# Kernel tuning notes

Hardware: AMD Instinct MI355X
Metric: run time of the kernel (lower is better)

Reference implementation:

```python
import jax, jax.numpy as jnp
import numpy as np

G, NPG, C, H, F, L = 256, 128, 16, 128, 128, 3
N = G * NPG          # 32768 nodes
E = 524288           # 16 edges per node on average
REG, REG_C = 0.01, 0.01
LN_EPS = 1e-5


def setup_inputs() -> dict:
    key = jax.random.key(0)
    ks = jax.random.split(key, 20)
    x = jax.random.normal(ks[0], (N, F), dtype=jnp.float32)
    # edges kept within each graph so dense pooling matches to_dense_batch semantics
    epg = E // G
    offs = jnp.repeat(jnp.arange(G, dtype=jnp.int64) * NPG, epg)
    src = jax.random.randint(ks[1], (E,), 0, NPG, dtype=jnp.int64) + offs
    tgt = jax.random.randint(ks[2], (E,), 0, NPG, dtype=jnp.int64) + offs
    edge_index = jnp.stack([src, tgt])
    mask_breaks = jax.random.bernoulli(ks[3], 0.5, (E,))
    s = jax.random.uniform(ks[4], (N, C), dtype=jnp.float32)
    batch = jnp.repeat(jnp.arange(G, dtype=jnp.int64), NPG)
    sc = 1.0 / np.sqrt(H)
    Wn = jax.random.normal(ks[5], (L, H, H), dtype=jnp.float32) * sc
    bn_ = jax.random.normal(ks[6], (L, H), dtype=jnp.float32) * sc
    Wo = jax.random.normal(ks[7], (L, H, H), dtype=jnp.float32) * sc
    bo = jax.random.normal(ks[8], (L, H), dtype=jnp.float32) * sc
    Wr = jax.random.normal(ks[9], (L, H, H), dtype=jnp.float32) * sc
    ln_g = jnp.ones((L, H), dtype=jnp.float32)
    ln_b = jnp.zeros((L, H), dtype=jnp.float32)
    fln_g = jnp.ones((H,), dtype=jnp.float32)
    fln_b = jnp.zeros((H,), dtype=jnp.float32)
    lin_w = jax.random.normal(ks[10], (1, H), dtype=jnp.float32) * sc
    bias = jnp.zeros((1,), dtype=jnp.float32)
    return {"x": x, "edge_index": edge_index, "mask_breaks": mask_breaks, "s": s,
            "batch": batch, "Wn": Wn, "bn_": bn_, "Wo": Wo, "bo": bo, "Wr": Wr,
            "ln_g": ln_g, "ln_b": ln_b, "fln_g": fln_g, "fln_b": fln_b,
            "lin_w": lin_w, "bias": bias}


def _layernorm(h, g, b):
    mu = jnp.mean(h, axis=-1, keepdims=True)
    v = jnp.mean(jnp.square(h - mu), axis=-1, keepdims=True)
    return (h - mu) * jax.lax.rsqrt(v + LN_EPS) * g + b


def reference(x, edge_index, mask_breaks, s, batch, Wn, bn_, Wo, bo, Wr,
              ln_g, ln_b, fln_g, fln_b, lin_w, bias):
    src, tgt = edge_index[0], edge_index[1]
    ones_e = jnp.ones((E,), dtype=x.dtype)
    cnt = jax.ops.segment_sum(ones_e, tgt, num_segments=N)          # in-degree
    inv_cnt = (1.0 / jnp.maximum(cnt, 1.0))[:, None]
    h = x
    for i in range(L):
        x_in = h @ Wn[i].T + bn_[i]
        x_out = h @ Wo[i].T + bo[i]
        x_root = h @ Wr[i].T
        msg = jnp.where(mask_breaks[:, None], x_in[src], x_out[src])  # [E,H]
        agg = jax.ops.segment_sum(msg, tgt, num_segments=N) * inv_cnt  # mean aggr
        h = jax.nn.relu(_layernorm(agg + x_root, ln_g[i], ln_b[i]))
    # dense per-graph views (equal-size graphs, batch ids sorted -> reshape)
    xd = h.reshape(G, NPG, H)
    sd = s.reshape(G, NPG, C)
    pooled = jnp.einsum("gnc,gnh->gch", sd, xd)                      # [G,C,H]
    pooled = _layernorm(pooled, fln_g, fln_b)
    xc = pooled @ lin_w.T                                            # [G,C,1]
    col_sum = sd.sum(axis=1)                                          # [G,C]
    cmask = (col_sum > 0)[..., None]
    xc = xc * cmask.astype(xc.dtype)
    out = xc.sum(axis=1) + bias                                      # [G,1]
    reg_loss = jnp.abs(Wo).sum() + jnp.abs(bo).sum()
    denom = (cmask.astype(xc.dtype).squeeze(-1) + 1e-7).sum(axis=1, keepdims=True)
    l1_loss = (jnp.abs(xc).sum(axis=1) / denom).mean()
    losses = REG * reg_loss + REG_C * l1_loss
    return out, losses, xc
```

## Files before the change

kernel.cpp:

```cpp
#include <hip/hip_runtime.h>

#define NN   32768
#define HD   128
#define EE   524288
#define GG   256
#define EPG  2048
#define CCd  16
#define LLd  3

typedef short short8 __attribute__((ext_vector_type(8)));
typedef float f32x4 __attribute__((ext_vector_type(4)));

__device__ __forceinline__ unsigned short f2bf(float f) {
  unsigned u = __builtin_bit_cast(unsigned, f);
  return (unsigned short)((u + 0x7FFFu + ((u >> 16) & 1u)) >> 16);
}
__device__ __forceinline__ unsigned bfpack(float a, float b) {
  return (unsigned)f2bf(a) | ((unsigned)f2bf(b) << 16);
}

__global__ __launch_bounds__(256) void convert_w_kernel(const float* __restrict__ Wn, const float* __restrict__ Wo,
                                                        const float* __restrict__ Wr, const float* __restrict__ bo,
                                                        unsigned* __restrict__ Wnb, unsigned* __restrict__ Wob,
                                                        unsigned* __restrict__ Wrb, float* __restrict__ wsreg) {
  int i = blockIdx.x * 256 + threadIdx.x;
  float4 a = *(const float4*)(Wn + (size_t)i * 4);
  float4 b = *(const float4*)(Wo + (size_t)i * 4);
  float4 c = *(const float4*)(Wr + (size_t)i * 4);
  *(uint2*)(Wnb + (size_t)i * 2) = make_uint2(bfpack(a.x, a.y), bfpack(a.z, a.w));
  *(uint2*)(Wob + (size_t)i * 2) = make_uint2(bfpack(b.x, b.y), bfpack(b.z, b.w));
  *(uint2*)(Wrb + (size_t)i * 2) = make_uint2(bfpack(c.x, c.y), bfpack(c.z, c.w));
  float s = fabsf(b.x) + fabsf(b.y) + fabsf(b.z) + fabsf(b.w);
  if (blockIdx.x == 0 && threadIdx.x < 96) {
    float4 d = *(const float4*)(bo + threadIdx.x * 4);
    s += fabsf(d.x) + fabsf(d.y) + fabsf(d.z) + fabsf(d.w);
  }
#pragma unroll
  for (int mk = 1; mk < 64; mk <<= 1) s += __shfl_xor(s, mk, 64);
  if ((threadIdx.x & 63) == 0) atomicAdd(wsreg, s);
}

__global__ __launch_bounds__(256) void build_m_kernel(const int* __restrict__ src, const int* __restrict__ tgt,
                                                      const int* __restrict__ mask,
                                                      unsigned* __restrict__ Mb, float* __restrict__ fin,
                                                      float* __restrict__ fout) {
  __shared__ unsigned Mi[2 * 128 * 64];
  const int g = blockIdx.x;
  const int tid = threadIdx.x;
  for (int i = tid; i < 16384; i += 256) Mi[i] = 0;
  __syncthreads();
  const int e0 = g * EPG;
#pragma unroll
  for (int i = 0; i < 8; ++i) {
    int e = e0 + i * 256 + tid;
    int t = tgt[e] & 127;
    int sl = src[e] & 127;
    int dir = (mask[e] != 0) ? 0 : 1;
    atomicAdd(&Mi[dir * 8192 + t * 64 + (sl >> 1)], 1u << ((sl & 1) * 16));
  }
  __syncthreads();
  const int t = tid >> 1, p = tid & 1;
  unsigned nin = 0, nout = 0;
#pragma unroll 4
  for (int k = 0; k < 32; ++k) { unsigned v = Mi[t * 64 + p * 32 + k]; nin += (v & 0xffffu) + (v >> 16); }
#pragma unroll 4
  for (int k = 0; k < 32; ++k) { unsigned v = Mi[8192 + t * 64 + p * 32 + k]; nout += (v & 0xffffu) + (v >> 16); }
  nin += __shfl_xor((int)nin, 1);
  nout += __shfl_xor((int)nout, 1);
  unsigned dg = nin + nout;
  float inv = 1.0f / (float)(dg > 0 ? dg : 1);
  if (p == 0) { fin[g * 128 + t] = (float)nin * inv; fout[g * 128 + t] = (float)nout * inv; }
#pragma unroll
  for (int dir = 0; dir < 2; ++dir) {
    int base = dir * 8192 + t * 64 + p * 32;
#pragma unroll
    for (int k4 = 0; k4 < 8; ++k4) {
      uint4 v = *(const uint4*)&Mi[base + k4 * 4];
      uint4 o;
      o.x = bfpack((float)(v.x & 0xffffu) * inv, (float)(v.x >> 16) * inv);
      o.y = bfpack((float)(v.y & 0xffffu) * inv, (float)(v.y >> 16) * inv);
      o.z = bfpack((float)(v.z & 0xffffu) * inv, (float)(v.z >> 16) * inv);
      o.w = bfpack((float)(v.w & 0xffffu) * inv, (float)(v.w >> 16) * inv);
      *(uint4*)&Mb[(size_t)g * 16384 + base + k4 * 4] = o;
    }
  }
}

#define SSTR 136
#define YSTR 40
__global__ __launch_bounds__(512) void fused_kernel(
    const float* __restrict__ x, const unsigned short* __restrict__ Mb,
    const unsigned short* __restrict__ Wnb, const unsigned short* __restrict__ Wob,
    const unsigned short* __restrict__ Wrb,
    const float* __restrict__ bn, const float* __restrict__ bo,
    const float* __restrict__ fin, const float* __restrict__ fout,
    const float* __restrict__ lng, const float* __restrict__ lnb,
    const float* __restrict__ s,
    const float* __restrict__ flng, const float* __restrict__ flnb,
    const float* __restrict__ linw, const float* __restrict__ bias,
    float* __restrict__ out, float* __restrict__ l1g) {
  __shared__ unsigned short scratch[128 * SSTR];
  __shared__ unsigned short ys[2 * 128 * YSTR];
  __shared__ unsigned short sTs[16 * SSTR];
  __shared__ float colsumS[CCd];
  __shared__ float xcs[CCd], axcs[CCd], msk[CCd];

  const int g = blockIdx.x;
  const int tid = threadIdx.x;
  const int wave = tid >> 6;
  const int lane = tid & 63;
  const int m = lane & 15;
  const int q = lane >> 4;
  const unsigned short* Mg = Mb + (size_t)g * 32768;
  unsigned* scratch32 = (unsigned*)scratch;

  {
    const float4* xg = (const float4*)(x + (size_t)g * 16384);
#pragma unroll
    for (int i = 0; i < 8; ++i) {
      int flat = i * 512 + tid;
      int t = flat >> 5, f = (flat & 31) << 2;
      float4 v = xg[flat];
      int w0 = (t * SSTR + f) >> 1;
      scratch32[w0] = bfpack(v.x, v.y);
      scratch32[w0 + 1] = bfpack(v.z, v.w);
    }
    int t = tid >> 2, c0 = (tid & 3) << 2;
    float4 v = *(const float4*)(s + (size_t)g * 2048 + t * 16 + c0);
    sTs[(c0 + 0) * SSTR + t] = f2bf(v.x);
    sTs[(c0 + 1) * SSTR + t] = f2bf(v.y);
    sTs[(c0 + 2) * SSTR + t] = f2bf(v.z);
    sTs[(c0 + 3) * SSTR + t] = f2bf(v.w);
    if (tid < CCd) {
      float cs = 0.f;
      for (int tt = 0; tt < 128; ++tt) cs += s[(size_t)g * 2048 + tt * 16 + tid];
      colsumS[tid] = cs;
    }
  }
  __syncthreads();

  for (int L = 0; L < LLd; ++L) {
    const unsigned short* WnL = Wnb + (size_t)L * 16384;
    const unsigned short* WoL = Wob + (size_t)L * 16384;
    const unsigned short* WrL = Wrb + (size_t)L * 16384;
    f32x4 pre[8];
#pragma unroll
    for (int ct = 0; ct < 8; ++ct) pre[ct] = (f32x4){0.f, 0.f, 0.f, 0.f};

#pragma unroll
    for (int ks = 0; ks < 4; ++ks) {
      short8 a = *(const short8*)&scratch[(wave * 16 + m) * SSTR + ks * 32 + q * 8];
#pragma unroll
      for (int ct = 0; ct < 8; ++ct) {
        short8 b = *(const short8*)(WrL + (size_t)(ct * 16 + m) * 128 + ks * 32 + q * 8);
        pre[ct] = __builtin_amdgcn_mfma_f32_16x16x32_bf16(a, b, pre[ct], 0, 0, 0);
      }
    }

    short8 wnf[4], wof[4];
#pragma unroll
    for (int ks = 0; ks < 4; ++ks) {
      wnf[ks] = *(const short8*)(WnL + (size_t)(wave * 16 + m) * 128 + ks * 32 + q * 8);
      wof[ks] = *(const short8*)(WoL + (size_t)(wave * 16 + m) * 128 + ks * 32 + q * 8);
    }

    for (int sc = 0; sc < 4; ++sc) {
      f32x4 ya[2][2];
#pragma unroll
      for (int o2 = 0; o2 < 2; ++o2)
#pragma unroll
        for (int st = 0; st < 2; ++st) ya[o2][st] = (f32x4){0.f, 0.f, 0.f, 0.f};
#pragma unroll
      for (int ks = 0; ks < 4; ++ks) {
        short8 a0 = *(const short8*)&scratch[(sc * 32 + m) * SSTR + ks * 32 + q * 8];
        short8 a1 = *(const short8*)&scratch[(sc * 32 + 16 + m) * SSTR + ks * 32 + q * 8];
        ya[0][0] = __builtin_amdgcn_mfma_f32_16x16x32_bf16(a0, wnf[ks], ya[0][0], 0, 0, 0);
        ya[0][1] = __builtin_amdgcn_mfma_f32_16x16x32_bf16(a1, wnf[ks], ya[0][1], 0, 0, 0);
        ya[1][0] = __builtin_amdgcn_mfma_f32_16x16x32_bf16(a0, wof[ks], ya[1][0], 0, 0, 0);
        ya[1][1] = __builtin_amdgcn_mfma_f32_16x16x32_bf16(a1, wof[ks], ya[1][1], 0, 0, 0);
      }
#pragma unroll
      for (int o2 = 0; o2 < 2; ++o2)
#pragma unroll
        for (int st = 0; st < 2; ++st)
#pragma unroll
          for (int r = 0; r < 4; ++r)
            ys[o2 * 128 * YSTR + (wave * 16 + m) * YSTR + st * 16 + q * 4 + r] = f2bf(ya[o2][st][r]);
      __syncthreads();
#pragma unroll
      for (int o2 = 0; o2 < 2; ++o2) {
        short8 am = *(const short8*)(Mg + (size_t)o2 * 16384 + (size_t)(wave * 16 + m) * 128 + sc * 32 + q * 8);
#pragma unroll
        for (int ct = 0; ct < 8; ++ct) {
          short8 b = *(const short8*)&ys[o2 * 128 * YSTR + (ct * 16 + m) * YSTR + q * 8];
          pre[ct] = __builtin_amdgcn_mfma_f32_16x16x32_bf16(am, b, pre[ct], 0, 0, 0);
        }
      }
      if (sc < 3) __syncthreads();
    }

    float bnv[8], bov[8], gv[8], bv[8];
#pragma unroll
    for (int ct = 0; ct < 8; ++ct) {
      int c = L * 128 + ct * 16 + m;
      bnv[ct] = bn[c]; bov[ct] = bo[c]; gv[ct] = lng[c]; bv[ct] = lnb[c];
    }
#pragma unroll
    for (int r = 0; r < 4; ++r) {
      const int tl = q * 4 + r;
      const int T = g * 128 + wave * 16 + tl;
      const float fiv = fin[T], fov = fout[T];
      float v[8];
      float sum = 0.f;
#pragma unroll
      for (int ct = 0; ct < 8; ++ct) {
        v[ct] = pre[ct][r] + fiv * bnv[ct] + fov * bov[ct];
        sum += v[ct];
      }
      sum += __shfl_xor(sum, 1); sum += __shfl_xor(sum, 2);
      sum += __shfl_xor(sum, 4); sum += __shfl_xor(sum, 8);
      const float mu = sum * (1.0f / 128.0f);
      float sq = 0.f;
#pragma unroll
      for (int ct = 0; ct < 8; ++ct) { float d = v[ct] - mu; sq += d * d; }
      sq += __shfl_xor(sq, 1); sq += __shfl_xor(sq, 2);
      sq += __shfl_xor(sq, 4); sq += __shfl_xor(sq, 8);
      const float rstd = rsqrtf(sq * (1.0f / 128.0f) + 1e-5f);
#pragma unroll
      for (int ct = 0; ct < 8; ++ct) {
        float o = fmaxf((v[ct] - mu) * rstd * gv[ct] + bv[ct], 0.0f);
        scratch[(wave * 16 + tl) * SSTR + ct * 16 + m] = f2bf(o);
      }
    }
    __syncthreads();
  }

  f32x4 pl = (f32x4){0.f, 0.f, 0.f, 0.f};
#pragma unroll
  for (int ks = 0; ks < 4; ++ks) {
    short8 a = *(const short8*)&sTs[m * SSTR + ks * 32 + q * 8];
    short8 b;
#pragma unroll
    for (int j = 0; j < 8; ++j)
      b[j] = (short)scratch[(ks * 32 + q * 8 + j) * SSTR + wave * 16 + m];
    pl = __builtin_amdgcn_mfma_f32_16x16x32_bf16(a, b, pl, 0, 0, 0);
  }
  float* pooledS = (float*)ys;
#pragma unroll
  for (int r = 0; r < 4; ++r) pooledS[(q * 4 + r) * 132 + wave * 16 + m] = pl[r];
  __syncthreads();

  if (tid < 256) {
    const int c = tid >> 4;
    const int j0 = (tid & 15) << 3;
    float v[8];
#pragma unroll
    for (int jj = 0; jj < 8; ++jj) v[jj] = pooledS[c * 132 + j0 + jj];
    float sum = 0.f;
#pragma unroll
    for (int jj = 0; jj < 8; ++jj) sum += v[jj];
#pragma unroll
    for (int mk = 1; mk < 16; mk <<= 1) sum += __shfl_xor(sum, mk, 64);
    float mu = sum * (1.0f / 128.0f);
    float sq = 0.f;
#pragma unroll
    for (int jj = 0; jj < 8; ++jj) { float d = v[jj] - mu; sq += d * d; }
#pragma unroll
    for (int mk = 1; mk < 16; mk <<= 1) sq += __shfl_xor(sq, mk, 64);
    float rstd = rsqrtf(sq * (1.0f / 128.0f) + 1e-5f);
    float dot = 0.f;
#pragma unroll
    for (int jj = 0; jj < 8; ++jj) {
      float nv = (v[jj] - mu) * rstd * flng[j0 + jj] + flnb[j0 + jj];
      dot += nv * linw[j0 + jj];
    }
#pragma unroll
    for (int mk = 1; mk < 16; mk <<= 1) dot += __shfl_xor(dot, mk, 64);
    if ((tid & 15) == 0) {
      float cm = (colsumS[c] > 0.f) ? 1.0f : 0.0f;
      float xcv = dot * cm;
      out[257 + g * CCd + c] = xcv;
      xcs[c] = xcv; axcs[c] = fabsf(xcv); msk[c] = cm;
    }
  }
  __syncthreads();
  if (tid == 0) {
    float so = 0.f, sa = 0.f, sd = 0.f;
#pragma unroll
    for (int k = 0; k < CCd; ++k) { so += xcs[k]; sa += axcs[k]; sd += msk[k] + 1e-7f; }
    out[g] = so + bias[0];
    l1g[g] = sa / sd;
  }
}

__global__ __launch_bounds__(256) void combine_kernel(const float* __restrict__ l1g, const float* __restrict__ wsreg,
                                                      float* __restrict__ outp) {
  const int tid = threadIdx.x;
  float s2 = l1g[tid];
#pragma unroll
  for (int mk = 1; mk < 64; mk <<= 1) s2 += __shfl_xor(s2, mk, 64);
  __shared__ float rs2[4];
  if ((tid & 63) == 0) rs2[tid >> 6] = s2;
  __syncthreads();
  if (tid == 0) {
    float l1 = (rs2[0] + rs2[1] + rs2[2] + rs2[3]) * (1.0f / GG);
    outp[0] = 0.01f * wsreg[0] + 0.01f * l1;
  }
}

extern "C" void kernel_launch(void* const* d_in, const int* in_sizes, int n_in,
                              void* d_out, int out_size, void* d_ws, size_t ws_size,
                              hipStream_t stream) {
  (void)in_sizes; (void)n_in; (void)out_size; (void)ws_size;
  const float* x    = (const float*)d_in[0];
  const int*   ei   = (const int*)d_in[1];
  const int*   mask = (const int*)d_in[2];
  const float* s    = (const float*)d_in[3];
  const float* Wn   = (const float*)d_in[5];
  const float* bn   = (const float*)d_in[6];
  const float* Wo   = (const float*)d_in[7];
  const float* bo   = (const float*)d_in[8];
  const float* Wr   = (const float*)d_in[9];
  const float* lng  = (const float*)d_in[10];
  const float* lnb  = (const float*)d_in[11];
  const float* flng = (const float*)d_in[12];
  const float* flnb = (const float*)d_in[13];
  const float* linw = (const float*)d_in[14];
  const float* bias = (const float*)d_in[15];
  float* out = (float*)d_out;

  char* ws = (char*)d_ws;
  size_t off = 0;
  auto alloc = [&](size_t b) { char* p = ws + off; off += (b + 255) & ~(size_t)255; return p; };
  unsigned short* Mbuf = (unsigned short*)alloc((size_t)GG * 2 * 128 * 128 * 2);
  float* fin    = (float*)alloc((size_t)NN * 4);
  float* fout   = (float*)alloc((size_t)NN * 4);
  unsigned short* Wnb = (unsigned short*)alloc((size_t)LLd * HD * HD * 2);
  unsigned short* Wob = (unsigned short*)alloc((size_t)LLd * HD * HD * 2);
  unsigned short* Wrb = (unsigned short*)alloc((size_t)LLd * HD * HD * 2);
  float* l1g    = (float*)alloc((size_t)GG * 4);
  float* wsreg  = (float*)alloc(256);

  const int* srcA = ei;
  const int* tgtA = ei + EE;

  hipMemsetAsync(wsreg, 0, 4, stream);
  convert_w_kernel<<<LLd * HD * HD / (256 * 4), 256, 0, stream>>>(Wn, Wo, Wr, bo,
      (unsigned*)Wnb, (unsigned*)Wob, (unsigned*)Wrb, wsreg);
  build_m_kernel<<<GG, 256, 0, stream>>>(srcA, tgtA, mask, (unsigned*)Mbuf, fin, fout);
  fused_kernel<<<GG, 512, 0, stream>>>(x, Mbuf, Wnb, Wob, Wrb, bn, bo, fin, fout,
                                       lng, lnb, s, flng, flnb, linw, bias, out, l1g);
  combine_kernel<<<1, 256, 0, stream>>>(l1g, wsreg, out + 256);
}
```

Measured before the change: 163.7 us.

## Merge prep kernels and split fused GNN work across 16 waves per graph

Folds the weight-conversion kernel into the adjacency-build kernel as extra blocks, which drops one launch. The per-graph fused kernel doubles to 1024 threads. Waves are split so half handle the Wn path and half the Wo path, and each half covers half of the output columns. LayerNorm statistics are now exchanged through shared memory using a single-pass sum and sum-of-squares. The adjacency build adds rotated LDS access to reduce bank conflicts, which costs more global stores. The higher thread count may hurt occupancy, and single-pass variance is slightly less accurate.

```diff
diff --git a/kernel.cpp b/kernel.cpp
--- a/kernel.cpp
+++ b/kernel.cpp
@@ -19,35 +19,37 @@
   return (unsigned)f2bf(a) | ((unsigned)f2bf(b) << 16);
 }
 
-__global__ __launch_bounds__(256) void convert_w_kernel(const float* __restrict__ Wn, const float* __restrict__ Wo,
-                                                        const float* __restrict__ Wr, const float* __restrict__ bo,
-                                                        unsigned* __restrict__ Wnb, unsigned* __restrict__ Wob,
-                                                        unsigned* __restrict__ Wrb, float* __restrict__ wsreg) {
-  int i = blockIdx.x * 256 + threadIdx.x;
-  float4 a = *(const float4*)(Wn + (size_t)i * 4);
-  float4 b = *(const float4*)(Wo + (size_t)i * 4);
-  float4 c = *(const float4*)(Wr + (size_t)i * 4);
-  *(uint2*)(Wnb + (size_t)i * 2) = make_uint2(bfpack(a.x, a.y), bfpack(a.z, a.w));
-  *(uint2*)(Wob + (size_t)i * 2) = make_uint2(bfpack(b.x, b.y), bfpack(b.z, b.w));
-  *(uint2*)(Wrb + (size_t)i * 2) = make_uint2(bfpack(c.x, c.y), bfpack(c.z, c.w));
-  float s = fabsf(b.x) + fabsf(b.y) + fabsf(b.z) + fabsf(b.w);
-  if (blockIdx.x == 0 && threadIdx.x < 96) {
-    float4 d = *(const float4*)(bo + threadIdx.x * 4);
-    s += fabsf(d.x) + fabsf(d.y) + fabsf(d.z) + fabsf(d.w);
-  }
-#pragma unroll
-  for (int mk = 1; mk < 64; mk <<= 1) s += __shfl_xor(s, mk, 64);
-  if ((threadIdx.x & 63) == 0) atomicAdd(wsreg, s);
-}
-
-__global__ __launch_bounds__(256) void build_m_kernel(const int* __restrict__ src, const int* __restrict__ tgt,
-                                                      const int* __restrict__ mask,
-                                                      unsigned* __restrict__ Mb, float* __restrict__ fin,
-                                                      float* __restrict__ fout) {
+__global__ __launch_bounds__(256) void prep_kernel(const int* __restrict__ src, const int* __restrict__ tgt,
+                                                   const int* __restrict__ mask,
+                                                   const float* __restrict__ Wn, const float* __restrict__ Wo,
+                                                   const float* __restrict__ Wr, const float* __restrict__ bo,
+                                                   unsigned* __restrict__ Mb, float* __restrict__ fin,
+                                                   float* __restrict__ fout,
+                                                   unsigned* __restrict__ Wnb, unsigned* __restrict__ Wob,
+                                                   unsigned* __restrict__ Wrb, float* __restrict__ wsreg) {
   __shared__ unsigned Mi[2 * 128 * 64];
+  const int tid = threadIdx.x;
+  if (blockIdx.x >= GG) {
+    int i = (blockIdx.x - GG) * 256 + tid;
+    float4 a = *(const float4*)(Wn + (size_t)i * 4);
+    float4 b = *(const float4*)(Wo + (size_t)i * 4);
+    float4 c = *(const float4*)(Wr + (size_t)i * 4);
+    *(uint2*)(Wnb + (size_t)i * 2) = make_uint2(bfpack(a.x, a.y), bfpack(a.z, a.w));
+    *(uint2*)(Wob + (size_t)i * 2) = make_uint2(bfpack(b.x, b.y), bfpack(b.z, b.w));
+    *(uint2*)(Wrb + (size_t)i * 2) = make_uint2(bfpack(c.x, c.y), bfpack(c.z, c.w));
+    float s = fabsf(b.x) + fabsf(b.y) + fabsf(b.z) + fabsf(b.w);
+    if (blockIdx.x == GG && tid < 96) {
+      float4 d = *(const float4*)(bo + tid * 4);
+      s += fabsf(d.x) + fabsf(d.y) + fabsf(d.z) + fabsf(d.w);
+    }
+#pragma unroll
+    for (int mk = 1; mk < 64; mk <<= 1) s += __shfl_xor(s, mk, 64);
+    if ((tid & 63) == 0) atomicAdd(wsreg, s);
+    return;
+  }
   const int g = blockIdx.x;
-  const int tid = threadIdx.x;
-  for (int i = tid; i < 16384; i += 256) Mi[i] = 0;
+  uint4* Mi4 = (uint4*)Mi;
+  for (int i = tid; i < 4096; i += 256) Mi4[i] = make_uint4(0, 0, 0, 0);
   __syncthreads();
   const int e0 = g * EPG;
 #pragma unroll
@@ -60,11 +62,12 @@
   }
   __syncthreads();
   const int t = tid >> 1, p = tid & 1;
+  const int b0 = t * 64 + p * 32;
   unsigned nin = 0, nout = 0;
-#pragma unroll 4
-  for (int k = 0; k < 32; ++k) { unsigned v = Mi[t * 64 + p * 32 + k]; nin += (v & 0xffffu) + (v >> 16); }
-#pragma unroll 4
-  for (int k = 0; k < 32; ++k) { unsigned v = Mi[8192 + t * 64 + p * 32 + k]; nout += (v & 0xffffu) + (v >> 16); }
+#pragma unroll 8
+  for (int k = 0; k < 32; ++k) { unsigned v = Mi[b0 + ((k + t) & 31)]; nin += (v & 0xffffu) + (v >> 16); }
+#pragma unroll 8
+  for (int k = 0; k < 32; ++k) { unsigned v = Mi[8192 + b0 + ((k + t) & 31)]; nout += (v & 0xffffu) + (v >> 16); }
   nin += __shfl_xor((int)nin, 1);
   nout += __shfl_xor((int)nout, 1);
   unsigned dg = nin + nout;
@@ -72,23 +75,19 @@
   if (p == 0) { fin[g * 128 + t] = (float)nin * inv; fout[g * 128 + t] = (float)nout * inv; }
 #pragma unroll
   for (int dir = 0; dir < 2; ++dir) {
-    int base = dir * 8192 + t * 64 + p * 32;
-#pragma unroll
-    for (int k4 = 0; k4 < 8; ++k4) {
-      uint4 v = *(const uint4*)&Mi[base + k4 * 4];
-      uint4 o;
-      o.x = bfpack((float)(v.x & 0xffffu) * inv, (float)(v.x >> 16) * inv);
-      o.y = bfpack((float)(v.y & 0xffffu) * inv, (float)(v.y >> 16) * inv);
-      o.z = bfpack((float)(v.z & 0xffffu) * inv, (float)(v.z >> 16) * inv);
-      o.w = bfpack((float)(v.w & 0xffffu) * inv, (float)(v.w >> 16) * inv);
-      *(uint4*)&Mb[(size_t)g * 16384 + base + k4 * 4] = o;
+    int base = dir * 8192 + b0;
+#pragma unroll 8
+    for (int k = 0; k < 32; ++k) {
+      int kk = (k + t) & 31;
+      unsigned v = Mi[base + kk];
+      Mb[(size_t)g * 16384 + base + kk] = bfpack((float)(v & 0xffffu) * inv, (float)(v >> 16) * inv);
     }
   }
 }
 
 #define SSTR 136
 #define YSTR 40
-__global__ __launch_bounds__(512) void fused_kernel(
+__global__ __launch_bounds__(1024) void fused_kernel(
     const float* __restrict__ x, const unsigned short* __restrict__ Mb,
     const unsigned short* __restrict__ Wnb, const unsigned short* __restrict__ Wob,
     const unsigned short* __restrict__ Wrb,
@@ -102,12 +101,15 @@
   __shared__ unsigned short scratch[128 * SSTR];
   __shared__ unsigned short ys[2 * 128 * YSTR];
   __shared__ unsigned short sTs[16 * SSTR];
+  __shared__ float pexch[128][4];
   __shared__ float colsumS[CCd];
   __shared__ float xcs[CCd], axcs[CCd], msk[CCd];
 
   const int g = blockIdx.x;
   const int tid = threadIdx.x;
   const int wave = tid >> 6;
+  const int h = wave >> 3;
+  const int w = wave & 7;
   const int lane = tid & 63;
   const int m = lane & 15;
   const int q = lane >> 4;
@@ -117,137 +119,146 @@
   {
     const float4* xg = (const float4*)(x + (size_t)g * 16384);
 #pragma unroll
-    for (int i = 0; i < 8; ++i) {
-      int flat = i * 512 + tid;
+    for (int i = 0; i < 4; ++i) {
+      int flat = i * 1024 + tid;
       int t = flat >> 5, f = (flat & 31) << 2;
       float4 v = xg[flat];
       int w0 = (t * SSTR + f) >> 1;
       scratch32[w0] = bfpack(v.x, v.y);
       scratch32[w0 + 1] = bfpack(v.z, v.w);
     }
-    int t = tid >> 2, c0 = (tid & 3) << 2;
-    float4 v = *(const float4*)(s + (size_t)g * 2048 + t * 16 + c0);
-    sTs[(c0 + 0) * SSTR + t] = f2bf(v.x);
-    sTs[(c0 + 1) * SSTR + t] = f2bf(v.y);
-    sTs[(c0 + 2) * SSTR + t] = f2bf(v.z);
-    sTs[(c0 + 3) * SSTR + t] = f2bf(v.w);
+    if (tid < 512) {
+      int t = tid >> 2, c0 = (tid & 3) << 2;
+      float4 v = *(const float4*)(s + (size_t)g * 2048 + t * 16 + c0);
+      sTs[(c0 + 0) * SSTR + t] = f2bf(v.x);
+      sTs[(c0 + 1) * SSTR + t] = f2bf(v.y);
+      sTs[(c0 + 2) * SSTR + t] = f2bf(v.z);
+      sTs[(c0 + 3) * SSTR + t] = f2bf(v.w);
+    }
     if (tid < CCd) {
       float cs = 0.f;
       for (int tt = 0; tt < 128; ++tt) cs += s[(size_t)g * 2048 + tt * 16 + tid];
       colsumS[tid] = cs;
     }
   }
+  float fivr[4], fovr[4];
+#pragma unroll
+  for (int r = 0; r < 4; ++r) {
+    fivr[r] = fin[g * 128 + w * 16 + q * 4 + r];
+    fovr[r] = fout[g * 128 + w * 16 + q * 4 + r];
+  }
   __syncthreads();
 
   for (int L = 0; L < LLd; ++L) {
     const unsigned short* WnL = Wnb + (size_t)L * 16384;
     const unsigned short* WoL = Wob + (size_t)L * 16384;
     const unsigned short* WrL = Wrb + (size_t)L * 16384;
-    f32x4 pre[8];
-#pragma unroll
-    for (int ct = 0; ct < 8; ++ct) pre[ct] = (f32x4){0.f, 0.f, 0.f, 0.f};
+    const unsigned short* Wh = h ? WoL : WnL;
+    short8 wf[4];
+#pragma unroll
+    for (int ks = 0; ks < 4; ++ks)
+      wf[ks] = *(const short8*)(Wh + (size_t)(w * 16 + m) * 128 + ks * 32 + q * 8);
+
+    f32x4 pre[4];
+#pragma unroll
+    for (int ct = 0; ct < 4; ++ct) pre[ct] = (f32x4){0.f, 0.f, 0.f, 0.f};
 
 #pragma unroll
     for (int ks = 0; ks < 4; ++ks) {
-      short8 a = *(const short8*)&scratch[(wave * 16 + m) * SSTR + ks * 32 + q * 8];
-#pragma unroll
-      for (int ct = 0; ct < 8; ++ct) {
-        short8 b = *(const short8*)(WrL + (size_t)(ct * 16 + m) * 128 + ks * 32 + q * 8);
+      short8 a = *(const short8*)&scratch[(w * 16 + m) * SSTR + ks * 32 + q * 8];
+#pragma unroll
+      for (int ct = 0; ct < 4; ++ct) {
+        short8 b = *(const short8*)(WrL + (size_t)((h * 4 + ct) * 16 + m) * 128 + ks * 32 + q * 8);
         pre[ct] = __builtin_amdgcn_mfma_f32_16x16x32_bf16(a, b, pre[ct], 0, 0, 0);
       }
     }
 
-    short8 wnf[4], wof[4];
-#pragma unroll
-    for (int ks = 0; ks < 4; ++ks) {
-      wnf[ks] = *(const short8*)(WnL + (size_t)(wave * 16 + m) * 128 + ks * 32 + q * 8);
-      wof[ks] = *(const short8*)(WoL + (size_t)(wave * 16 + m) * 128 + ks * 32 + q * 8);
-    }
-
     for (int sc = 0; sc < 4; ++sc) {
-      f32x4 ya[2][2];
-#pragma unroll
-      for (int o2 = 0; o2 < 2; ++o2)
-#pragma unroll
-        for (int st = 0; st < 2; ++st) ya[o2][st] = (f32x4){0.f, 0.f, 0.f, 0.f};
+      short8 am0 = *(const short8*)(Mg + (size_t)(w * 16 + m) * 128 + sc * 32 + q * 8);
+      short8 am1 = *(const short8*)(Mg + 16384 + (size_t)(w * 16 + m) * 128 + sc * 32 + q * 8);
+      f32x4 ya0 = (f32x4){0.f, 0.f, 0.f, 0.f}, ya1 = (f32x4){0.f, 0.f, 0.f, 0.f};
 #pragma unroll
       for (int ks = 0; ks < 4; ++ks) {
         short8 a0 = *(const short8*)&scratch[(sc * 32 + m) * SSTR + ks * 32 + q * 8];
         short8 a1 = *(const short8*)&scratch[(sc * 32 + 16 + m) * SSTR + ks * 32 + q * 8];
-        ya[0][0] = __builtin_amdgcn_mfma_f32_16x16x32_bf16(a0, wnf[ks], ya[0][0], 0, 0, 0);
-        ya[0][1] = __builtin_amdgcn_mfma_f32_16x16x32_bf16(a1, wnf[ks], ya[0][1], 0, 0, 0);
-        ya[1][0] = __builtin_amdgcn_mfma_f32_16x16x32_bf16(a0, wof[ks], ya[1][0], 0, 0, 0);
-        ya[1][1] = __builtin_amdgcn_mfma_f32_16x16x32_bf16(a1, wof[ks], ya[1][1], 0, 0, 0);
-      }
-#pragma unroll
-      for (int o2 = 0; o2 < 2; ++o2)
-#pragma unroll
-        for (int st = 0; st < 2; ++st)
-#pragma unroll
-          for (int r = 0; r < 4; ++r)
-            ys[o2 * 128 * YSTR + (wave * 16 + m) * YSTR + st * 16 + q * 4 + r] = f2bf(ya[o2][st][r]);
+        ya0 = __builtin_amdgcn_mfma_f32_16x16x32_bf16(a0, wf[ks], ya0, 0, 0, 0);
+        ya1 = __builtin_amdgcn_mfma_f32_16x16x32_bf16(a1, wf[ks], ya1, 0, 0, 0);
+      }
+      {
+        const int ybase = h * 128 * YSTR + (w * 16 + m) * YSTR + q * 4;
+#pragma unroll
+        for (int r = 0; r < 4; ++r) ys[ybase + r] = f2bf(ya0[r]);
+#pragma unroll
+        for (int r = 0; r < 4; ++r) ys[ybase + 16 + r] = f2bf(ya1[r]);
+      }
       __syncthreads();
 #pragma unroll
-      for (int o2 = 0; o2 < 2; ++o2) {
-        short8 am = *(const short8*)(Mg + (size_t)o2 * 16384 + (size_t)(wave * 16 + m) * 128 + sc * 32 + q * 8);
-#pragma unroll
-        for (int ct = 0; ct < 8; ++ct) {
-          short8 b = *(const short8*)&ys[o2 * 128 * YSTR + (ct * 16 + m) * YSTR + q * 8];
-          pre[ct] = __builtin_amdgcn_mfma_f32_16x16x32_bf16(am, b, pre[ct], 0, 0, 0);
-        }
+      for (int ct = 0; ct < 4; ++ct) {
+        short8 b0 = *(const short8*)&ys[((h * 4 + ct) * 16 + m) * YSTR + q * 8];
+        short8 b1 = *(const short8*)&ys[128 * YSTR + ((h * 4 + ct) * 16 + m) * YSTR + q * 8];
+        pre[ct] = __builtin_amdgcn_mfma_f32_16x16x32_bf16(am0, b0, pre[ct], 0, 0, 0);
+        pre[ct] = __builtin_amdgcn_mfma_f32_16x16x32_bf16(am1, b1, pre[ct], 0, 0, 0);
       }
       if (sc < 3) __syncthreads();
     }
 
-    float bnv[8], bov[8], gv[8], bv[8];
-#pragma unroll
-    for (int ct = 0; ct < 8; ++ct) {
-      int c = L * 128 + ct * 16 + m;
+    float bnv[4], bov[4], gv[4], bv[4];
+#pragma unroll
+    for (int ct = 0; ct < 4; ++ct) {
+      int c = L * 128 + (h * 4 + ct) * 16 + m;
       bnv[ct] = bn[c]; bov[ct] = bo[c]; gv[ct] = lng[c]; bv[ct] = lnb[c];
     }
+    float v[4][4];
 #pragma unroll
     for (int r = 0; r < 4; ++r) {
-      const int tl = q * 4 + r;
-      const int T = g * 128 + wave * 16 + tl;
-      const float fiv = fin[T], fov = fout[T];
-      float v[8];
-      float sum = 0.f;
-#pragma unroll
-      for (int ct = 0; ct < 8; ++ct) {
-        v[ct] = pre[ct][r] + fiv * bnv[ct] + fov * bov[ct];
-        sum += v[ct];
-      }
-      sum += __shfl_xor(sum, 1); sum += __shfl_xor(sum, 2);
-      sum += __shfl_xor(sum, 4); sum += __shfl_xor(sum, 8);
-      const float mu = sum * (1.0f / 128.0f);
-      float sq = 0.f;
-#pragma unroll
-      for (int ct = 0; ct < 8; ++ct) { float d = v[ct] - mu; sq += d * d; }
-      sq += __shfl_xor(sq, 1); sq += __shfl_xor(sq, 2);
-      sq += __shfl_xor(sq, 4); sq += __shfl_xor(sq, 8);
-      const float rstd = rsqrtf(sq * (1.0f / 128.0f) + 1e-5f);
-#pragma unroll
-      for (int ct = 0; ct < 8; ++ct) {
-        float o = fmaxf((v[ct] - mu) * rstd * gv[ct] + bv[ct], 0.0f);
-        scratch[(wave * 16 + tl) * SSTR + ct * 16 + m] = f2bf(o);
+      float sum = 0.f, sq = 0.f;
+#pragma unroll
+      for (int ct = 0; ct < 4; ++ct) {
+        float vv = pre[ct][r] + fivr[r] * bnv[ct] + fovr[r] * bov[ct];
+        v[r][ct] = vv;
+        sum += vv; sq += vv * vv;
+      }
+      sum += __shfl_xor(sum, 1); sq += __shfl_xor(sq, 1);
+      sum += __shfl_xor(sum, 2); sq += __shfl_xor(sq, 2);
+      sum += __shfl_xor(sum, 4); sq += __shfl_xor(sq, 4);
+      sum += __shfl_xor(sum, 8); sq += __shfl_xor(sq, 8);
+      if (m == 0) {
+        pexch[w * 16 + q * 4 + r][h * 2] = sum;
+        pexch[w * 16 + q * 4 + r][h * 2 + 1] = sq;
       }
     }
     __syncthreads();
-  }
-
-  f32x4 pl = (f32x4){0.f, 0.f, 0.f, 0.f};
-#pragma unroll
-  for (int ks = 0; ks < 4; ++ks) {
-    short8 a = *(const short8*)&sTs[m * SSTR + ks * 32 + q * 8];
-    short8 b;
-#pragma unroll
-    for (int j = 0; j < 8; ++j)
-      b[j] = (short)scratch[(ks * 32 + q * 8 + j) * SSTR + wave * 16 + m];
-    pl = __builtin_amdgcn_mfma_f32_16x16x32_bf16(a, b, pl, 0, 0, 0);
-  }
+#pragma unroll
+    for (int r = 0; r < 4; ++r) {
+      const int tl = w * 16 + q * 4 + r;
+      float4 px = *(const float4*)&pexch[tl][0];
+      float mu = (px.x + px.z) * (1.0f / 128.0f);
+      float var = (px.y + px.w) * (1.0f / 128.0f) - mu * mu;
+      float rstd = rsqrtf(fmaxf(var, 0.0f) + 1e-5f);
+#pragma unroll
+      for (int ct = 0; ct < 4; ++ct) {
+        float o = fmaxf((v[r][ct] - mu) * rstd * gv[ct] + bv[ct], 0.0f);
+        scratch[tl * SSTR + (h * 4 + ct) * 16 + m] = f2bf(o);
+      }
+    }
+    __syncthreads();
+  }
+
   float* pooledS = (float*)ys;
-#pragma unroll
-  for (int r = 0; r < 4; ++r) pooledS[(q * 4 + r) * 132 + wave * 16 + m] = pl[r];
+  if (h == 0) {
+    f32x4 pl = (f32x4){0.f, 0.f, 0.f, 0.f};
+#pragma unroll
+    for (int ks = 0; ks < 4; ++ks) {
+      short8 a = *(const short8*)&sTs[m * SSTR + ks * 32 + q * 8];
+      short8 b;
+#pragma unroll
+      for (int j = 0; j < 8; ++j)
+        b[j] = (short)scratch[(ks * 32 + q * 8 + j) * SSTR + w * 16 + m];
+      pl = __builtin_amdgcn_mfma_f32_16x16x32_bf16(a, b, pl, 0, 0, 0);
+    }
+#pragma unroll
+    for (int r = 0; r < 4; ++r) pooledS[(q * 4 + r) * 132 + w * 16 + m] = pl[r];
+  }
   __syncthreads();
 
   if (tid < 256) {
@@ -345,10 +356,9 @@
   const int* tgtA = ei + EE;
 
   hipMemsetAsync(wsreg, 0, 4, stream);
-  convert_w_kernel<<<LLd * HD * HD / (256 * 4), 256, 0, stream>>>(Wn, Wo, Wr, bo,
-      (unsigned*)Wnb, (unsigned*)Wob, (unsigned*)Wrb, wsreg);
-  build_m_kernel<<<GG, 256, 0, stream>>>(srcA, tgtA, mask, (unsigned*)Mbuf, fin, fout);
-  fused_kernel<<<GG, 512, 0, stream>>>(x, Mbuf, Wnb, Wob, Wrb, bn, bo, fin, fout,
-                                       lng, lnb, s, flng, flnb, linw, bias, out, l1g);
+  prep_kernel<<<GG + 48, 256, 0, stream>>>(srcA, tgtA, mask, Wn, Wo, Wr, bo,
+      (unsigned*)Mbuf, fin, fout, (unsigned*)Wnb, (unsigned*)Wob, (unsigned*)Wrb, wsreg);
+  fused_kernel<<<GG, 1024, 0, stream>>>(x, Mbuf, Wnb, Wob, Wrb, bn, bo, fin, fout,
+                                        lng, lnb, s, flng, flnb, linw, bias, out, l1g);
   combine_kernel<<<1, 256, 0, stream>>>(l1g, wsreg, out + 256);
 }
```

New measurement: 198.2 us. 21.1% more time.
